# Kernel tuning notes

Hardware: AMD Instinct MI355X
Metric: run time of the kernel (lower is better)

## Reference

```python
import jax, jax.numpy as jnp
import numpy as np

B, N, D, H = 2, 2048, 1024, 16
DH = D // H
SCALE = 1.0 / np.sqrt(DH).astype(np.float32)


def setup_inputs() -> dict:
    key = jax.random.key(0)
    k1, k2, k3, k4, k5 = jax.random.split(key, 5)
    x = jax.random.normal(k1, (B, N, D), dtype=jnp.float32)
    attn_bias = jax.random.normal(k2, (B, N, N), dtype=jnp.float32)
    # valid lengths in [N//2, N]; True = keep
    lengths = jax.random.randint(k3, (B,), N // 2, N + 1)
    key_padding_mask = jnp.arange(N)[None, :] < lengths[:, None]
    Wqkv = jax.random.normal(k4, (3 * D, D), dtype=jnp.float32) / np.sqrt(D)
    Wproj = jax.random.normal(k5, (D, D), dtype=jnp.float32) / np.sqrt(D)
    bproj = jnp.zeros((D,), dtype=jnp.float32)
    return {"x": x, "attn_bias": attn_bias, "key_padding_mask": key_padding_mask,
            "Wqkv": Wqkv, "Wproj": Wproj, "bproj": bproj}


def reference(x, attn_bias, key_padding_mask, Wqkv, Wproj, bproj):
    b, n, d = x.shape
    qkv = x @ Wqkv.T                                   # [B,N,3D]
    qkv = qkv.reshape(b, n, 3, H, DH)
    q = jnp.transpose(qkv[:, :, 0], (0, 2, 1, 3))      # [B,H,N,DH]
    k = jnp.transpose(qkv[:, :, 1], (0, 2, 1, 3))
    v = jnp.transpose(qkv[:, :, 2], (0, 2, 1, 3))
    attn = jnp.einsum('bhnd,bhmd->bhnm', q, k) * SCALE  # [B,H,N,N]
    attn = attn + attn_bias[:, None, :, :]
    attn = jnp.where(key_padding_mask[:, None, None, :], attn, -jnp.inf)
    attn = jax.nn.softmax(attn, axis=-1)
    y = jnp.einsum('bhnm,bhmd->bhnd', attn, v)          # [B,H,N,DH]
    y = jnp.transpose(y, (0, 2, 1, 3)).reshape(b, n, d)
    return y @ Wproj.T + bproj
```

## Files before the change

### kernel.cpp

```cpp
#include <hip/hip_runtime.h>
#include <hip/hip_bf16.h>

namespace {

typedef short short8 __attribute__((ext_vector_type(8)));
typedef float f32x4 __attribute__((ext_vector_type(4)));

#define L2E 1.4426950408889634f
#define SB() __builtin_amdgcn_sched_barrier(0)

__device__ __forceinline__ unsigned short f2bf(float f) {
  union { __hip_bfloat16 h; unsigned short u; } cv;
  cv.h = __float2bfloat16(f);
  return cv.u;
}

__device__ __forceinline__ unsigned cvt_pk_bf16(float lo, float hi) {
  unsigned r;
  asm("v_cvt_pk_bf16_f32 %0, %1, %2" : "=v"(r) : "v"(lo), "v"(hi));
  return r;
}

__device__ __forceinline__ void load_lds16(const void* g, void* l) {
  __builtin_amdgcn_global_load_lds((__attribute__((address_space(1))) void*)g,
                                   (__attribute__((address_space(3))) void*)l,
                                   16, 0, 0);
}

__device__ __forceinline__ int pi64(int rho) {
  const int c32 = rho & 32;
  const int o = (rho >> 4) & 1;
  const int g = (rho >> 2) & 3;
  const int s = rho & 3;
  return c32 + (o ? (((g ^ 2) << 3) + 4 + s) : ((g << 3) + s));
}

__global__ __launch_bounds__(256) void cvt_all(const float4* __restrict__ x,
                                               const float4* __restrict__ wqkv,
                                               const float4* __restrict__ wproj,
                                               ushort4* __restrict__ xb,
                                               ushort4* __restrict__ wqkvb,
                                               ushort4* __restrict__ wprojb) {
  const int base = blockIdx.x * 256 + threadIdx.x;
#pragma unroll
  for (int j = 0; j < 4; ++j) {
    const int i = base + j * 524288;
    const float4* src;
    ushort4* dst;
    int off;
    if (i < 1048576) { src = x; dst = xb; off = i; }
    else if (i < 1048576 + 786432) { src = wqkv; dst = wqkvb; off = i - 1048576; }
    else { src = wproj; dst = wprojb; off = i - (1048576 + 786432); }
    float4 f = src[off];
    ushort4 u;
    u.x = f2bf(f.x); u.y = f2bf(f.y); u.z = f2bf(f.z); u.w = f2bf(f.w);
    dst[off] = u;
  }
}

__global__ __launch_bounds__(256) void gemm_qkv(const unsigned short* __restrict__ Xb,
                                                const unsigned short* __restrict__ Wb,
                                                unsigned short* __restrict__ qws,
                                                unsigned short* __restrict__ kws,
                                                unsigned short* __restrict__ vTws) {
  __shared__ unsigned short lA[128 * 32];
  __shared__ unsigned short lB[128 * 32];
  const int t = threadIdx.x;
  const int w = t >> 6, l = t & 63;
  const int wm = w >> 1, wn = w & 1;
  const int lr = l & 15, lg = l >> 4;
  const int row0 = blockIdx.x * 128, col0 = blockIdx.y * 128;
  const int srow = t >> 2;
  const int schunk = (t & 3) ^ (srow & 3);
  f32x4 acc[4][4] = {};
  for (int k0 = 0; k0 < 1024; k0 += 32) {
    __syncthreads();
    load_lds16(Xb + (size_t)(row0 + srow) * 1024 + k0 + schunk * 8, &lA[w * 512]);
    load_lds16(Xb + (size_t)(row0 + 64 + srow) * 1024 + k0 + schunk * 8, &lA[2048 + w * 512]);
    load_lds16(Wb + (size_t)(col0 + srow) * 1024 + k0 + schunk * 8, &lB[w * 512]);
    load_lds16(Wb + (size_t)(col0 + 64 + srow) * 1024 + k0 + schunk * 8, &lB[2048 + w * 512]);
    __syncthreads();
    short8 af[4], bf[4];
    const int rslot = (lg ^ (l & 3)) * 8;
#pragma unroll
    for (int mi = 0; mi < 4; ++mi)
      af[mi] = *(const short8*)&lA[(wm * 64 + mi * 16 + lr) * 32 + rslot];
#pragma unroll
    for (int ni = 0; ni < 4; ++ni)
      bf[ni] = *(const short8*)&lB[(wn * 64 + ni * 16 + lr) * 32 + rslot];
#pragma unroll
    for (int mi = 0; mi < 4; ++mi)
#pragma unroll
      for (int ni = 0; ni < 4; ++ni)
        acc[mi][ni] = __builtin_amdgcn_mfma_f32_16x16x32_bf16(af[mi], bf[ni], acc[mi][ni], 0, 0, 0);
  }
#pragma unroll
  for (int mi = 0; mi < 4; ++mi)
#pragma unroll
    for (int ni = 0; ni < 4; ++ni) {
      const int col = col0 + wn * 64 + ni * 16 + lr;
      const int s = col >> 10, rem = col & 1023;
      const int hh = rem >> 6, dh = rem & 63;
      const int row = row0 + wm * 64 + mi * 16 + lg * 4;
      const int bb = row >> 11, n = row & 2047;
      const size_t bh = (size_t)(bb * 16 + hh);
      if (s == 2) {
        ushort4 u4;
        u4.x = f2bf(acc[mi][ni][0]); u4.y = f2bf(acc[mi][ni][1]);
        u4.z = f2bf(acc[mi][ni][2]); u4.w = f2bf(acc[mi][ni][3]);
        *(ushort4*)&vTws[(bh * 64 + dh) * 2048 + n] = u4;
      } else if (s == 0) {
#pragma unroll
        for (int r = 0; r < 4; ++r)
          qws[(bh * 2048 + n + r) * 64 + dh] = f2bf(acc[mi][ni][r] * 0.18033688011112042f);
      } else {
#pragma unroll
        for (int r = 0; r < 4; ++r)
          kws[(bh * 2048 + n + r) * 64 + dh] = f2bf(acc[mi][ni][r]);
      }
    }
}

__global__ __launch_bounds__(256, 4) void attn_fwd(const unsigned short* __restrict__ qws,
                                                   const unsigned short* __restrict__ kws,
                                                   const unsigned short* __restrict__ vTws,
                                                   const float* __restrict__ bias,
                                                   const int* __restrict__ mask,
                                                   unsigned short* __restrict__ ctx) {
  __shared__ unsigned short lK[2][64 * 64];
  __shared__ unsigned short lVT[2][64 * 64];
  const int t = threadIdx.x, w = t >> 6, l = t & 63;
  const int lr = l & 15, lg = l >> 4;
  const int xr7 = lr & 7;

  const int lin = blockIdx.x;
  const int xcd = lin & 7;
  const int u = (lin >> 3) & 63;
  const int b = lin >> 9;
  const int h = u & 15;
  const int qt = xcd * 4 + (u >> 4);

  const size_t bh = (size_t)(b * 16 + h);
  const unsigned short* Q = qws + bh * (2048 * 64);
  const unsigned short* K = kws + bh * (2048 * 64);
  const unsigned short* VT = vTws + bh * (64 * 2048);

  const int4* m4 = (const int4*)(mask + b * 2048);
  int scnt = 0;
#pragma unroll
  for (int i = 0; i < 8; ++i) {
    int4 v = m4[l + i * 64];
    scnt += (v.x != 0) + (v.y != 0) + (v.z != 0) + (v.w != 0);
  }
#pragma unroll
  for (int d = 1; d < 64; d <<= 1) scnt += __shfl_xor(scnt, d, 64);
  const int len = scnt;
  const int nt = ((((len + 63) >> 6) + 1) & ~1);

  const int qv = qt * 64 + w * 16 + lr;
  const short8 qf0 = *(const short8*)&Q[(size_t)qv * 64 + lg * 8];
  const short8 qf1 = *(const short8*)&Q[(size_t)qv * 64 + 32 + lg * 8];
  const float* bq = bias + (size_t)b * (2048 * 2048) + (size_t)qv * 2048;

  const int be = lg * 8, bo = ((lg ^ 2) * 8) + 4;
  const int boffs[4] = {be, bo, 32 + be, 32 + bo};

  short8 vones;
#pragma unroll
  for (int i = 0; i < 8; ++i) vones[i] = (short)0x3F80;

  f32x4 o[5] = {};

  const int sr = l >> 3;
  const int sc = ((l & 7) ^ sr) * 8;

  auto STAGE = [&](int ti2) {
    const int slot = ti2 & 1;
    const int kt2 = ti2 << 6;
#pragma unroll
    for (int u2 = 0; u2 < 2; ++u2) {
      const int row = w * 16 + u2 * 8 + sr;
      load_lds16(K + (size_t)(kt2 + pi64(row)) * 64 + sc, &lK[slot][(w * 16 + u2 * 8) * 64]);
      load_lds16(VT + (size_t)row * 2048 + kt2 + sc, &lVT[slot][(w * 16 + u2 * 8) * 64]);
    }
  };
  auto LOADB = [&](float4 (&d)[4], int ti2) {
    const int kt2 = ti2 << 6;
#pragma unroll
    for (int j = 0; j < 4; ++j) d[j] = *(const float4*)&bq[kt2 + boffs[j]];
  };
  auto COMPUTE = [&](int ti, float4 (&b4)[4], bool hn2) {
    const int slot = ti & 1;
    const int kt = ti << 6;
    const unsigned short* lKs = lK[slot];
    const unsigned short* lVs = lVT[slot];
    f32x4 s4[4];
    __builtin_amdgcn_s_setprio(1);
#pragma unroll
    for (int j = 0; j < 4; ++j) {
      f32x4 sj = {-16.f, -16.f, -16.f, -16.f};
      const int krow = (j * 16 + lr) * 64;
      short8 kf0 = *(const short8*)&lKs[krow + (lg ^ xr7) * 8];
      short8 kf1 = *(const short8*)&lKs[krow + ((lg + 4) ^ xr7) * 8];
      sj = __builtin_amdgcn_mfma_f32_16x16x32_bf16(kf0, qf0, sj, 0, 0, 0);
      sj = __builtin_amdgcn_mfma_f32_16x16x32_bf16(kf1, qf1, sj, 0, 0, 0);
      s4[j] = sj;
    }
    __builtin_amdgcn_s_setprio(0);
    if (kt + 64 <= len) {
#pragma unroll
      for (int j = 0; j < 4; ++j) {
        s4[j][0] = fmaf(b4[j].x, L2E, s4[j][0]);
        s4[j][1] = fmaf(b4[j].y, L2E, s4[j][1]);
        s4[j][2] = fmaf(b4[j].z, L2E, s4[j][2]);
        s4[j][3] = fmaf(b4[j].w, L2E, s4[j][3]);
      }
    } else {
#pragma unroll
      for (int j = 0; j < 4; ++j) {
        const int kb = kt + boffs[j];
        const float* bp = &b4[j].x;
#pragma unroll
        for (int r = 0; r < 4; ++r)
          s4[j][r] = (kb + r < len) ? fmaf(bp[r], L2E, s4[j][r]) : -1e30f;
      }
    }
    if (hn2) LOADB(b4, ti + 2);
#pragma unroll
    for (int j = 0; j < 4; ++j)
#pragma unroll
      for (int r = 0; r < 4; ++r) s4[j][r] = __builtin_amdgcn_exp2f(s4[j][r]);
    unsigned wj0[4], wj1[4];
#pragma unroll
    for (int j = 0; j < 4; ++j) {
      wj0[j] = cvt_pk_bf16(s4[j][0], s4[j][1]);
      wj1[j] = cvt_pk_bf16(s4[j][2], s4[j][3]);
    }
#pragma unroll
    for (int c = 0; c < 2; ++c) {
      union { unsigned u4a[4]; short8 s8; } pu;
      pu.u4a[0] = wj0[2 * c];
      pu.u4a[1] = wj1[2 * c];
      pu.u4a[2] = (unsigned)__shfl_xor((int)wj0[2 * c + 1], 32, 64);
      pu.u4a[3] = (unsigned)__shfl_xor((int)wj1[2 * c + 1], 32, 64);
      __builtin_amdgcn_s_setprio(1);
#pragma unroll
      for (int ni = 0; ni < 4; ++ni) {
        short8 vf = *(const short8*)&lVs[(ni * 16 + lr) * 64 + ((c * 4 + lg) ^ xr7) * 8];
        o[ni] = __builtin_amdgcn_mfma_f32_16x16x32_bf16(pu.s8, vf, o[ni], 0, 0, 0);
      }
      o[4] = __builtin_amdgcn_mfma_f32_16x16x32_bf16(pu.s8, vones, o[4], 0, 0, 0);
      __builtin_amdgcn_s_setprio(0);
    }
  };

  float4 bA[4], bB[4];
  SB();
  STAGE(0);
  SB();
  LOADB(bA, 0);
  LOADB(bB, 1);
  SB();
  asm volatile("s_waitcnt vmcnt(4)" ::: "memory");
  __builtin_amdgcn_s_barrier();
  SB();

  for (int ti = 0; ti < nt; ti += 2) {
    const bool h2 = (ti + 2 < nt);
    SB();
    STAGE(ti + 1);
    SB();
    COMPUTE(ti, bA, h2);
    SB();
    asm volatile("s_waitcnt vmcnt(4) lgkmcnt(0)" ::: "memory");
    __builtin_amdgcn_s_barrier();
    SB();
    if (h2) { STAGE(ti + 2); SB(); }
    COMPUTE(ti + 1, bB, h2);
    if (h2) {
      SB();
      asm volatile("s_waitcnt vmcnt(4) lgkmcnt(0)" ::: "memory");
      __builtin_amdgcn_s_barrier();
      SB();
    }
  }

  float linv[4];
#pragma unroll
  for (int r = 0; r < 4; ++r) linv[r] = __builtin_amdgcn_rcpf(o[4][r]);
#pragma unroll
  for (int r = 0; r < 4; ++r) {
    const size_t orow = (size_t)b * 2048 + qt * 64 + w * 16 + lg * 4 + r;
#pragma unroll
    for (int ni = 0; ni < 4; ++ni)
      ctx[orow * 1024 + h * 64 + ni * 16 + lr] = f2bf(o[ni][r] * linv[r]);
  }
}

__global__ __launch_bounds__(256) void gemm_proj(const unsigned short* __restrict__ Cb,
                                                 const unsigned short* __restrict__ Wb,
                                                 const float* __restrict__ bproj,
                                                 float* __restrict__ out) {
  __shared__ unsigned short lA[128 * 32];
  __shared__ unsigned short lB[128 * 32];
  const int t = threadIdx.x;
  const int w = t >> 6, l = t & 63;
  const int wm = w >> 1, wn = w & 1;
  const int lr = l & 15, lg = l >> 4;
  const int row0 = blockIdx.x * 128, col0 = blockIdx.y * 128;
  const int srow = t >> 2;
  const int schunk = (t & 3) ^ (srow & 3);
  f32x4 acc[4][4] = {};
  for (int k0 = 0; k0 < 1024; k0 += 32) {
    __syncthreads();
    load_lds16(Cb + (size_t)(row0 + srow) * 1024 + k0 + schunk * 8, &lA[w * 512]);
    load_lds16(Cb + (size_t)(row0 + 64 + srow) * 1024 + k0 + schunk * 8, &lA[2048 + w * 512]);
    load_lds16(Wb + (size_t)(col0 + srow) * 1024 + k0 + schunk * 8, &lB[w * 512]);
    load_lds16(Wb + (size_t)(col0 + 64 + srow) * 1024 + k0 + schunk * 8, &lB[2048 + w * 512]);
    __syncthreads();
    short8 af[4], bf[4];
    const int rslot = (lg ^ (l & 3)) * 8;
#pragma unroll
    for (int mi = 0; mi < 4; ++mi)
      af[mi] = *(const short8*)&lA[(wm * 64 + mi * 16 + lr) * 32 + rslot];
#pragma unroll
    for (int ni = 0; ni < 4; ++ni)
      bf[ni] = *(const short8*)&lB[(wn * 64 + ni * 16 + lr) * 32 + rslot];
#pragma unroll
    for (int mi = 0; mi < 4; ++mi)
#pragma unroll
      for (int ni = 0; ni < 4; ++ni)
        acc[mi][ni] = __builtin_amdgcn_mfma_f32_16x16x32_bf16(af[mi], bf[ni], acc[mi][ni], 0, 0, 0);
  }
#pragma unroll
  for (int mi = 0; mi < 4; ++mi)
#pragma unroll
    for (int ni = 0; ni < 4; ++ni) {
      const int col = col0 + wn * 64 + ni * 16 + lr;
      const float bp = bproj[col];
#pragma unroll
      for (int r = 0; r < 4; ++r) {
        const int row = row0 + wm * 64 + mi * 16 + lg * 4 + r;
        out[(size_t)row * 1024 + col] = acc[mi][ni][r] + bp;
      }
    }
}

}

extern "C" void kernel_launch(void* const* d_in, const int* in_sizes, int n_in,
                              void* d_out, int out_size, void* d_ws, size_t ws_size,
                              hipStream_t stream) {
  (void)in_sizes; (void)n_in; (void)out_size; (void)ws_size;
  const float* x        = (const float*)d_in[0];
  const float* attnbias = (const float*)d_in[1];
  const int*   mask     = (const int*)d_in[2];
  const float* Wqkv     = (const float*)d_in[3];
  const float* Wproj    = (const float*)d_in[4];
  const float* bproj    = (const float*)d_in[5];
  float* out = (float*)d_out;

  unsigned short* ws     = (unsigned short*)d_ws;
  unsigned short* xb     = ws;
  unsigned short* wqkvb  = xb + 4194304;
  unsigned short* wprojb = wqkvb + 3145728;
  unsigned short* qws    = wprojb + 1048576;
  unsigned short* kws    = qws + 4194304;
  unsigned short* vTws   = kws + 4194304;
  unsigned short* ctxb   = vTws + 4194304;

  cvt_all<<<2048, 256, 0, stream>>>((const float4*)x, (const float4*)Wqkv,
                                    (const float4*)Wproj, (ushort4*)xb,
                                    (ushort4*)wqkvb, (ushort4*)wprojb);
  gemm_qkv<<<dim3(32, 24), 256, 0, stream>>>(xb, wqkvb, qws, kws, vTws);
  attn_fwd<<<1024, 256, 0, stream>>>(qws, kws, vTws, attnbias, mask, ctxb);
  gemm_proj<<<dim3(32, 8), 256, 0, stream>>>(ctxb, wprojb, bproj, out);
}
```

Baseline: 148.5 us.

## Split attention over two key halves and merge partials in a combine kernel

```diff
diff --git a/kernel.cpp b/kernel.cpp
--- a/kernel.cpp
+++ b/kernel.cpp
@@ -27,12 +27,8 @@
                                    16, 0, 0);
 }
 
-__device__ __forceinline__ int pi64(int rho) {
-  const int c32 = rho & 32;
-  const int o = (rho >> 4) & 1;
-  const int g = (rho >> 2) & 3;
-  const int s = rho & 3;
-  return c32 + (o ? (((g ^ 2) << 3) + 4 + s) : ((g << 3) + s));
+__device__ __forceinline__ int pi32(int rho) {
+  return ((rho >> 2) & 3) * 8 + ((rho >> 4) & 1) * 4 + (rho & 3);
 }
 
 __global__ __launch_bounds__(256) void cvt_all(const float4* __restrict__ x,
@@ -121,24 +117,26 @@
     }
 }
 
-__global__ __launch_bounds__(256, 4) void attn_fwd(const unsigned short* __restrict__ qws,
+__global__ __launch_bounds__(256, 8) void attn_fwd(const unsigned short* __restrict__ qws,
                                                    const unsigned short* __restrict__ kws,
                                                    const unsigned short* __restrict__ vTws,
                                                    const float* __restrict__ bias,
                                                    const int* __restrict__ mask,
-                                                   unsigned short* __restrict__ ctx) {
-  __shared__ unsigned short lK[2][64 * 64];
-  __shared__ unsigned short lVT[2][64 * 64];
+                                                   unsigned short* __restrict__ pO,
+                                                   float* __restrict__ pS) {
+  __shared__ unsigned short lK[2][32 * 64];
+  __shared__ unsigned short lVT[2][64 * 32];
   const int t = threadIdx.x, w = t >> 6, l = t & 63;
   const int lr = l & 15, lg = l >> 4;
   const int xr7 = lr & 7;
 
   const int lin = blockIdx.x;
   const int xcd = lin & 7;
-  const int u = (lin >> 3) & 63;
-  const int b = lin >> 9;
-  const int h = u & 15;
-  const int qt = xcd * 4 + (u >> 4);
+  const int half = (lin >> 8) & 1;
+  const int b = (lin >> 9) & 1;
+  const int uu = ((lin >> 3) & 31) | (((lin >> 10) & 1) << 5);
+  const int h = uu & 15;
+  const int qt = xcd * 4 + (uu >> 4);
 
   const size_t bh = (size_t)(b * 16 + h);
   const unsigned short* Q = qws + bh * (2048 * 64);
@@ -155,15 +153,15 @@
 #pragma unroll
   for (int d = 1; d < 64; d <<= 1) scnt += __shfl_xor(scnt, d, 64);
   const int len = scnt;
-  const int nt = ((((len + 63) >> 6) + 1) & ~1);
+  const int kt0 = half << 10;
+  const int nt = half ? (((((len - 1024) + 31) >> 5) + 1) & ~1) : 32;
 
   const int qv = qt * 64 + w * 16 + lr;
   const short8 qf0 = *(const short8*)&Q[(size_t)qv * 64 + lg * 8];
   const short8 qf1 = *(const short8*)&Q[(size_t)qv * 64 + 32 + lg * 8];
   const float* bq = bias + (size_t)b * (2048 * 2048) + (size_t)qv * 2048;
 
-  const int be = lg * 8, bo = ((lg ^ 2) * 8) + 4;
-  const int boffs[4] = {be, bo, 32 + be, 32 + bo};
+  const int be = lg * 8;
 
   short8 vones;
 #pragma unroll
@@ -171,33 +169,31 @@
 
   f32x4 o[5] = {};
 
-  const int sr = l >> 3;
-  const int sc = ((l & 7) ^ sr) * 8;
+  const int skr = l >> 3;
+  const int sck = ((l & 7) ^ skr) * 8;
+  const int svr = l >> 2;
+  const int scv = ((l & 3) ^ ((l >> 3) & 3)) * 8;
 
   auto STAGE = [&](int ti2) {
     const int slot = ti2 & 1;
-    const int kt2 = ti2 << 6;
-#pragma unroll
-    for (int u2 = 0; u2 < 2; ++u2) {
-      const int row = w * 16 + u2 * 8 + sr;
-      load_lds16(K + (size_t)(kt2 + pi64(row)) * 64 + sc, &lK[slot][(w * 16 + u2 * 8) * 64]);
-      load_lds16(VT + (size_t)row * 2048 + kt2 + sc, &lVT[slot][(w * 16 + u2 * 8) * 64]);
-    }
+    const int kt2 = kt0 + (ti2 << 5);
+    load_lds16(K + (size_t)(kt2 + pi32(w * 8 + skr)) * 64 + sck, &lK[slot][w * 512]);
+    load_lds16(VT + (size_t)(w * 16 + svr) * 2048 + kt2 + scv, &lVT[slot][w * 512]);
   };
-  auto LOADB = [&](float4 (&d)[4], int ti2) {
-    const int kt2 = ti2 << 6;
-#pragma unroll
-    for (int j = 0; j < 4; ++j) d[j] = *(const float4*)&bq[kt2 + boffs[j]];
+  auto LOADB = [&](float4 (&d)[2], int ti2) {
+    const int kt2 = kt0 + (ti2 << 5);
+    d[0] = *(const float4*)&bq[kt2 + be];
+    d[1] = *(const float4*)&bq[kt2 + be + 4];
   };
-  auto COMPUTE = [&](int ti, float4 (&b4)[4], bool hn2) {
+  auto COMPUTE = [&](int ti, float4 (&b4)[2], bool hn2) {
     const int slot = ti & 1;
-    const int kt = ti << 6;
+    const int kt = kt0 + (ti << 5);
     const unsigned short* lKs = lK[slot];
     const unsigned short* lVs = lVT[slot];
-    f32x4 s4[4];
+    f32x4 s4[2];
     __builtin_amdgcn_s_setprio(1);
 #pragma unroll
-    for (int j = 0; j < 4; ++j) {
+    for (int j = 0; j < 2; ++j) {
       f32x4 sj = {-16.f, -16.f, -16.f, -16.f};
       const int krow = (j * 16 + lr) * 64;
       short8 kf0 = *(const short8*)&lKs[krow + (lg ^ xr7) * 8];
@@ -207,9 +203,9 @@
       s4[j] = sj;
     }
     __builtin_amdgcn_s_setprio(0);
-    if (kt + 64 <= len) {
-#pragma unroll
-      for (int j = 0; j < 4; ++j) {
+    if (kt + 32 <= len) {
+#pragma unroll
+      for (int j = 0; j < 2; ++j) {
         s4[j][0] = fmaf(b4[j].x, L2E, s4[j][0]);
         s4[j][1] = fmaf(b4[j].y, L2E, s4[j][1]);
         s4[j][2] = fmaf(b4[j].z, L2E, s4[j][2]);
@@ -217,8 +213,8 @@
       }
     } else {
 #pragma unroll
-      for (int j = 0; j < 4; ++j) {
-        const int kb = kt + boffs[j];
+      for (int j = 0; j < 2; ++j) {
+        const int kb = kt + be + j * 4;
         const float* bp = &b4[j].x;
 #pragma unroll
         for (int r = 0; r < 4; ++r)
@@ -227,74 +223,90 @@
     }
     if (hn2) LOADB(b4, ti + 2);
 #pragma unroll
-    for (int j = 0; j < 4; ++j)
+    for (int j = 0; j < 2; ++j)
 #pragma unroll
       for (int r = 0; r < 4; ++r) s4[j][r] = __builtin_amdgcn_exp2f(s4[j][r]);
-    unsigned wj0[4], wj1[4];
-#pragma unroll
-    for (int j = 0; j < 4; ++j) {
-      wj0[j] = cvt_pk_bf16(s4[j][0], s4[j][1]);
-      wj1[j] = cvt_pk_bf16(s4[j][2], s4[j][3]);
-    }
-#pragma unroll
-    for (int c = 0; c < 2; ++c) {
-      union { unsigned u4a[4]; short8 s8; } pu;
-      pu.u4a[0] = wj0[2 * c];
-      pu.u4a[1] = wj1[2 * c];
-      pu.u4a[2] = (unsigned)__shfl_xor((int)wj0[2 * c + 1], 32, 64);
-      pu.u4a[3] = (unsigned)__shfl_xor((int)wj1[2 * c + 1], 32, 64);
-      __builtin_amdgcn_s_setprio(1);
-#pragma unroll
-      for (int ni = 0; ni < 4; ++ni) {
-        short8 vf = *(const short8*)&lVs[(ni * 16 + lr) * 64 + ((c * 4 + lg) ^ xr7) * 8];
-        o[ni] = __builtin_amdgcn_mfma_f32_16x16x32_bf16(pu.s8, vf, o[ni], 0, 0, 0);
-      }
-      o[4] = __builtin_amdgcn_mfma_f32_16x16x32_bf16(pu.s8, vones, o[4], 0, 0, 0);
-      __builtin_amdgcn_s_setprio(0);
-    }
+    union { unsigned u4a[4]; short8 s8; } pu;
+    pu.u4a[0] = cvt_pk_bf16(s4[0][0], s4[0][1]);
+    pu.u4a[1] = cvt_pk_bf16(s4[0][2], s4[0][3]);
+    pu.u4a[2] = cvt_pk_bf16(s4[1][0], s4[1][1]);
+    pu.u4a[3] = cvt_pk_bf16(s4[1][2], s4[1][3]);
+    __builtin_amdgcn_s_setprio(1);
+#pragma unroll
+    for (int ni = 0; ni < 4; ++ni) {
+      short8 vf = *(const short8*)&lVs[(ni * 16 + lr) * 32 + ((lg ^ ((lr >> 1) & 3))) * 8];
+      o[ni] = __builtin_amdgcn_mfma_f32_16x16x32_bf16(pu.s8, vf, o[ni], 0, 0, 0);
+    }
+    o[4] = __builtin_amdgcn_mfma_f32_16x16x32_bf16(pu.s8, vones, o[4], 0, 0, 0);
+    __builtin_amdgcn_s_setprio(0);
   };
 
-  float4 bA[4], bB[4];
-  SB();
-  STAGE(0);
-  SB();
-  LOADB(bA, 0);
-  LOADB(bB, 1);
-  SB();
-  asm volatile("s_waitcnt vmcnt(4)" ::: "memory");
-  __builtin_amdgcn_s_barrier();
-  SB();
-
-  for (int ti = 0; ti < nt; ti += 2) {
-    const bool h2 = (ti + 2 < nt);
+  if (nt > 0) {
+    float4 bA[2], bB[2];
     SB();
-    STAGE(ti + 1);
+    STAGE(0);
     SB();
-    COMPUTE(ti, bA, h2);
+    LOADB(bA, 0);
+    LOADB(bB, 1);
     SB();
-    asm volatile("s_waitcnt vmcnt(4) lgkmcnt(0)" ::: "memory");
+    asm volatile("s_waitcnt vmcnt(2)" ::: "memory");
     __builtin_amdgcn_s_barrier();
     SB();
-    if (h2) { STAGE(ti + 2); SB(); }
-    COMPUTE(ti + 1, bB, h2);
-    if (h2) {
+
+    for (int ti = 0; ti < nt; ti += 2) {
+      const bool h2 = (ti + 2 < nt);
       SB();
-      asm volatile("s_waitcnt vmcnt(4) lgkmcnt(0)" ::: "memory");
+      STAGE(ti + 1);
+      SB();
+      COMPUTE(ti, bA, h2);
+      SB();
+      if (h2) asm volatile("s_waitcnt vmcnt(2) lgkmcnt(0)" ::: "memory");
+      else    asm volatile("s_waitcnt vmcnt(0) lgkmcnt(0)" ::: "memory");
       __builtin_amdgcn_s_barrier();
       SB();
-    }
-  }
-
-  float linv[4];
-#pragma unroll
-  for (int r = 0; r < 4; ++r) linv[r] = __builtin_amdgcn_rcpf(o[4][r]);
+      if (h2) { STAGE(ti + 2); SB(); }
+      COMPUTE(ti + 1, bB, h2);
+      if (h2) {
+        SB();
+        asm volatile("s_waitcnt vmcnt(2) lgkmcnt(0)" ::: "memory");
+        __builtin_amdgcn_s_barrier();
+        SB();
+      }
+    }
+  }
+
+  const size_t pbase = (size_t)(half * 32) + bh;
 #pragma unroll
   for (int r = 0; r < 4; ++r) {
-    const size_t orow = (size_t)b * 2048 + qt * 64 + w * 16 + lg * 4 + r;
+    const int q = qt * 64 + w * 16 + lg * 4 + r;
+    const size_t ob = (pbase * 2048 + q) * 64;
 #pragma unroll
     for (int ni = 0; ni < 4; ++ni)
-      ctx[orow * 1024 + h * 64 + ni * 16 + lr] = f2bf(o[ni][r] * linv[r]);
-  }
+      pO[ob + ni * 16 + lr] = f2bf(o[ni][r]);
+    if (lr == 0) pS[pbase * 2048 + q] = o[4][r];
+  }
+}
+
+__global__ __launch_bounds__(256) void combine(const unsigned short* __restrict__ pO,
+                                               const float* __restrict__ pS,
+                                               unsigned short* __restrict__ ctx) {
+  const int id = blockIdx.x * 256 + threadIdx.x;
+  const int dh4 = id & 15;
+  const int n = (id >> 4) & 2047;
+  const int bh = id >> 15;
+  const size_t i0 = ((size_t)bh * 2048 + n) * 64 + dh4 * 4;
+  const size_t i1 = ((size_t)(32 + bh) * 2048 + n) * 64 + dh4 * 4;
+  ushort4 lo = *(const ushort4*)&pO[i0];
+  ushort4 hi = *(const ushort4*)&pO[i1];
+  const float s = pS[(size_t)bh * 2048 + n] + pS[(size_t)(32 + bh) * 2048 + n];
+  const float inv = __builtin_amdgcn_rcpf(s);
+  ushort4 u;
+  u.x = f2bf((__uint_as_float((unsigned)lo.x << 16) + __uint_as_float((unsigned)hi.x << 16)) * inv);
+  u.y = f2bf((__uint_as_float((unsigned)lo.y << 16) + __uint_as_float((unsigned)hi.y << 16)) * inv);
+  u.z = f2bf((__uint_as_float((unsigned)lo.z << 16) + __uint_as_float((unsigned)hi.z << 16)) * inv);
+  u.w = f2bf((__uint_as_float((unsigned)lo.w << 16) + __uint_as_float((unsigned)hi.w << 16)) * inv);
+  const int b = bh >> 4, h = bh & 15;
+  *(ushort4*)&ctx[((size_t)b * 2048 + n) * 1024 + h * 64 + dh4 * 4] = u;
 }
 
 __global__ __launch_bounds__(256) void gemm_proj(const unsigned short* __restrict__ Cb,
@@ -368,11 +380,14 @@
   unsigned short* kws    = qws + 4194304;
   unsigned short* vTws   = kws + 4194304;
   unsigned short* ctxb   = vTws + 4194304;
+  unsigned short* pO     = ctxb + 4194304;
+  float* pS = (float*)xb;
 
   cvt_all<<<2048, 256, 0, stream>>>((const float4*)x, (const float4*)Wqkv,
                                     (const float4*)Wproj, (ushort4*)xb,
                                     (ushort4*)wqkvb, (ushort4*)wprojb);
   gemm_qkv<<<dim3(32, 24), 256, 0, stream>>>(xb, wqkvb, qws, kws, vTws);
-  attn_fwd<<<1024, 256, 0, stream>>>(qws, kws, vTws, attnbias, mask, ctxb);
+  attn_fwd<<<2048, 256, 0, stream>>>(qws, kws, vTws, attnbias, mask, pO, pS);
+  combine<<<4096, 256, 0, stream>>>(pO, pS, ctxb);
   gemm_proj<<<dim3(32, 8), 256, 0, stream>>>(ctxb, wprojb, bproj, out);
 }
```

Result: slower. 388.9 us (+161.8%).
